# Kernel optimization log

Hardware: AMD Instinct MI355X
Metric: run time of the kernel (lower is better)

The kernel has to match this reference:

```python
import jax, jax.numpy as jnp
import numpy as np
from jax import lax

DIM = 256
HEADS = 8
B, H, W = 8, 128, 128
EPS_LN = 1e-5
EPS_NORM = 1e-12


def _ln(x, w, b):
    # WithBias LayerNorm over channel dim, x: [b,c,h,w]
    mu = x.mean(axis=1, keepdims=True)
    var = ((x - mu) ** 2).mean(axis=1, keepdims=True)
    return (x - mu) / jnp.sqrt(var + EPS_LN) * w[None, :, None, None] + b[None, :, None, None]


def _conv1x1(x, w, b):
    # w: [out,in]
    return jnp.einsum('bchw,oc->bohw', x, w) + b[None, :, None, None]


def _dwconv3(x, w, b=None):
    # depthwise 3x3, w: [C,1,3,3]
    c = x.shape[1]
    y = lax.conv_general_dilated(x, w, (1, 1), 'SAME',
                                 dimension_numbers=('NCHW', 'OIHW', 'NCHW'),
                                 feature_group_count=c)
    if b is not None:
        y = y + b[None, :, None, None]
    return y


def setup_inputs() -> dict:
    key = jax.random.key(0)
    ks = jax.random.split(key, 10)
    s = 0.02
    return {
        'x': jax.random.normal(ks[0], (B, DIM, H, W), jnp.float32),
        'hx': jax.random.normal(ks[1], (B, DIM, H, W), jnp.float32),
        'ln1_w': jnp.ones((DIM,), jnp.float32),
        'ln1_b': jnp.zeros((DIM,), jnp.float32),
        'ln2_w': jnp.ones((DIM,), jnp.float32),
        'ln2_b': jnp.zeros((DIM,), jnp.float32),
        'q_w': jax.random.normal(ks[2], (DIM, DIM), jnp.float32) * s,
        'q_b': jnp.zeros((DIM,), jnp.float32),
        'q_dw_w': jax.random.normal(ks[3], (DIM, 1, 3, 3), jnp.float32) * s,
        'q_dw_b': jnp.zeros((DIM,), jnp.float32),
        'kv_w': jax.random.normal(ks[4], (2 * DIM, DIM), jnp.float32) * s,
        'kv_b': jnp.zeros((2 * DIM,), jnp.float32),
        'kv_dw_w': jax.random.normal(ks[5], (2 * DIM, 1, 3, 3), jnp.float32) * s,
        'kv_dw_b': jnp.zeros((2 * DIM,), jnp.float32),
        'ao_w': jax.random.normal(ks[6], (DIM, DIM), jnp.float32) * s,
        'ao_b': jnp.zeros((DIM,), jnp.float32),
        'pe1_w': jax.random.normal(ks[7], (DIM, 1, 3, 3), jnp.float32) * s,
        'pe2_w': jax.random.normal(ks[8], (DIM, 1, 3, 3), jnp.float32) * s,
        'temperature': jnp.ones((HEADS, 1, 1), jnp.float32),
    }


def reference(x, hx, ln1_w, ln1_b, ln2_w, ln2_b, q_w, q_b, q_dw_w, q_dw_b,
              kv_w, kv_b, kv_dw_w, kv_dw_b, ao_w, ao_b, pe1_w, pe2_w, temperature):
    b, c, h, w = hx.shape
    q = _dwconv3(_conv1x1(_ln(x, ln1_w, ln1_b), q_w, q_b), q_dw_w, q_dw_b)
    kv = _dwconv3(_conv1x1(_ln(hx, ln2_w, ln2_b), kv_w, kv_b), kv_dw_w, kv_dw_b)
    k, v = jnp.split(kv, 2, axis=1)
    # positional embedding branch: dwconv -> GELU -> dwconv (no bias)
    p_emb = _dwconv3(jax.nn.gelu(_dwconv3(v, pe1_w)), pe2_w)
    hd = c // HEADS
    # [b, head, hd, hw]
    qh = q.reshape(b, HEADS, hd, h * w)
    kh = k.reshape(b, HEADS, hd, h * w)
    vh = v.reshape(b, HEADS, hd, h * w)
    qh = qh / jnp.maximum(jnp.linalg.norm(qh, axis=-1, keepdims=True), EPS_NORM)
    kh = kh / jnp.maximum(jnp.linalg.norm(kh, axis=-1, keepdims=True), EPS_NORM)
    attn = jnp.einsum('bhcn,bhdn->bhcd', qh, kh) * temperature[None]
    attn = jax.nn.softmax(attn, axis=-1)
    out = jnp.einsum('bhcd,bhdn->bhcn', attn, vh).reshape(b, c, h, w)
    return _conv1x1(out, ao_w, ao_b) + p_emb + hx
```

## Files before the change

### kernel.cpp

```cpp
#include <hip/hip_runtime.h>
#include <cstdio>
#include <cstdint>

typedef unsigned short u16;
typedef short short8 __attribute__((ext_vector_type(8)));
typedef float floatx4 __attribute__((ext_vector_type(4)));

#define NPIX 16384
#define DIM 256

__device__ inline float bf2f(u16 v) {
    return __uint_as_float(((uint32_t)v) << 16);
}
__device__ inline u16 f2bf(float f) {
    uint32_t u = __float_as_uint(f);
    u += 0x7fffu + ((u >> 16) & 1u);
    return (u16)(u >> 16);
}
__device__ inline float gelu_tanh(float x) {
    float x3 = x * x * x;
    return 0.5f * x * (1.f + tanhf(0.7978845608028654f * (x + 0.044715f * x3)));
}
__device__ inline void load8(const u16* p, size_t idx, int isf32, float out[8]) {
    if (isf32) {
        const float4* f = (const float4*)((const float*)p + idx);
        float4 a = f[0], b = f[1];
        out[0] = a.x; out[1] = a.y; out[2] = a.z; out[3] = a.w;
        out[4] = b.x; out[5] = b.y; out[6] = b.z; out[7] = b.w;
    } else {
        uint4 d = *(const uint4*)(p + idx);
        u16 v[8]; *(uint4*)v = d;
#pragma unroll
        for (int j = 0; j < 8; ++j) out[j] = bf2f(v[j]);
    }
}

__global__ __launch_bounds__(256)
void detect_dtype(const u16* __restrict__ x, int* __restrict__ flag) {
    __shared__ int sh[256];
    int t = threadIdx.x;
    const uint32_t* w = (const uint32_t*)x;
    int cnt = 0;
    for (int i = t; i < 4096; i += 256) {
        int e = (w[i] >> 7) & 0xFF;
        if (e >= 110 && e <= 134) cnt++;
    }
    sh[t] = cnt;
    __syncthreads();
    if (t == 0) {
        int s = 0;
        for (int i = 0; i < 256; ++i) s += sh[i];
        *flag = (s < 2048) ? 1 : 0;
    }
}

struct WArgs {
    const void* src[17];
    int off[17];
    int n[17];
};
__global__ __launch_bounds__(256)
void convert_params(WArgs a, const int* __restrict__ flag, u16* __restrict__ dst) {
    int isf32 = *flag;
    int w = blockIdx.y;
    const void* s = a.src[w];
    u16* d = dst + a.off[w];
    int n = a.n[w];
    for (int i = blockIdx.x * 256 + threadIdx.x; i < n; i += gridDim.x * 256)
        d[i] = isf32 ? f2bf(((const float*)s)[i]) : ((const u16*)s)[i];
}

__global__ __launch_bounds__(256)
void ln_stats(const u16* __restrict__ x, const int* __restrict__ flag,
              float* __restrict__ mu, float* __restrict__ rstd) {
    int isf32 = *flag;
    int g = blockIdx.x * 256 + threadIdx.x;
    int b = g >> 14, n = g & (NPIX - 1);
    float s = 0.f, s2 = 0.f;
    if (isf32) {
        const float* p = (const float*)x + (size_t)b * DIM * NPIX + n;
        for (int c = 0; c < DIM; ++c) { float v = p[(size_t)c * NPIX]; s += v; s2 += v * v; }
    } else {
        const u16* p = x + (size_t)b * DIM * NPIX + n;
        for (int c = 0; c < DIM; ++c) { float v = bf2f(p[(size_t)c * NPIX]); s += v; s2 += v * v; }
    }
    float m = s * (1.f / 256.f);
    float var = s2 * (1.f / 256.f) - m * m;
    mu[g] = m;
    rstd[g] = rsqrtf(var + 1e-5f);
}

__global__ __launch_bounds__(256)
void ln_transpose(const u16* __restrict__ x, const int* __restrict__ flag,
                  const float* __restrict__ mu, const float* __restrict__ rstd,
                  const u16* __restrict__ lnw, const u16* __restrict__ lnb,
                  u16* __restrict__ xt) {
    int isf32 = *flag;
    __shared__ u16 T[64][72];
    int b = blockIdx.x >> 8;
    int n0 = (blockIdx.x & 255) * 64;
    int c0 = blockIdx.y * 64;
    int t = threadIdx.x;
#pragma unroll
    for (int l = 0; l < 2; ++l) {
        int idx = t + l * 256;
        int cl = idx >> 3, nch = (idx & 7) * 8;
        float vals[8];
        load8(x, ((size_t)(b * DIM + c0 + cl)) * NPIX + n0 + nch, isf32, vals);
        float w = bf2f(lnw[c0 + cl]), bb = bf2f(lnb[c0 + cl]);
#pragma unroll
        for (int j = 0; j < 8; ++j) {
            int g = b * NPIX + n0 + nch + j;
            float v = (vals[j] - mu[g]) * rstd[g] * w + bb;
            T[nch + j][cl] = f2bf(v);
        }
    }
    __syncthreads();
#pragma unroll
    for (int l = 0; l < 2; ++l) {
        int idx = t + l * 256;
        int nl = idx >> 3, cch = (idx & 7) * 8;
        uint4 d = *(const uint4*)&T[nl][cch];
        *(uint4*)(xt + (size_t)(b * NPIX + n0 + nl) * DIM + c0 + cch) = d;
    }
}

template <int HAS_ADD>
__global__ __launch_bounds__(256)
void gemm_bf16(const u16* __restrict__ A, const u16* __restrict__ Bw,
               const u16* __restrict__ bias, const u16* __restrict__ addt,
               u16* __restrict__ C, int ldc) {
    __shared__ u16 As[128][40];
    __shared__ u16 Bs[128][40];
    const int m0 = blockIdx.x * 128;
    const int n0 = blockIdx.y * 128;
    const int t = threadIdx.x;
    const int lane = t & 63;
    const int wid = t >> 6;
    const int wm = (wid >> 1) * 64;
    const int wn = (wid & 1) * 64;
    const int frow = lane & 15;
    const int koff = (lane >> 4) * 8;
    floatx4 acc[4][4] = {};
    for (int k0 = 0; k0 < 256; k0 += 32) {
#pragma unroll
        for (int l = 0; l < 2; ++l) {
            int idx = t + l * 256;
            int r = idx >> 2, ch = (idx & 3) * 8;
            *(uint4*)&As[r][ch] = *(const uint4*)(A + (size_t)(m0 + r) * 256 + k0 + ch);
            *(uint4*)&Bs[r][ch] = *(const uint4*)(Bw + (size_t)(n0 + r) * 256 + k0 + ch);
        }
        __syncthreads();
        short8 af[4], bfr[4];
#pragma unroll
        for (int i = 0; i < 4; ++i) {
            af[i] = *(const short8*)&As[wm + i * 16 + frow][koff];
            bfr[i] = *(const short8*)&Bs[wn + i * 16 + frow][koff];
        }
#pragma unroll
        for (int i = 0; i < 4; ++i)
#pragma unroll
            for (int j = 0; j < 4; ++j)
                acc[i][j] = __builtin_amdgcn_mfma_f32_16x16x32_bf16(af[i], bfr[j], acc[i][j], 0, 0, 0);
        __syncthreads();
    }
    const int col = lane & 15;
    const int r0 = (lane >> 4) * 4;
#pragma unroll
    for (int j = 0; j < 4; ++j) {
        int o = n0 + wn + j * 16 + col;
        float bv = bf2f(bias[o]);
#pragma unroll
        for (int i = 0; i < 4; ++i) {
#pragma unroll
            for (int r = 0; r < 4; ++r) {
                int m = m0 + wm + i * 16 + r0 + r;
                size_t off = (size_t)m * ldc + o;
                float v = acc[i][j][r] + bv;
                if (HAS_ADD) v += bf2f(addt[off]);
                C[off] = f2bf(v);
            }
        }
    }
}

__global__ __launch_bounds__(256)
void dwconv3_nhwc(const u16* __restrict__ in, int in_stride, int in_off,
                  const u16* __restrict__ w9, const u16* __restrict__ bias,
                  u16* __restrict__ out, int out_stride, int out_off,
                  int C, int do_gelu) {
    extern __shared__ float wsm[];
    int t = threadIdx.x;
    for (int i = t; i < C * 9; i += 256) {
        int c = i / 9, tap = i % 9;
        wsm[tap * C + c] = bf2f(w9[i]);
    }
    __syncthreads();
    const int tpp = C >> 3;
    const int ppb = 256 / tpp;
    int pix = blockIdx.x * ppb + t / tpp;
    int c8 = (t % tpp) * 8;
    int b = pix >> 14, n = pix & (NPIX - 1);
    int y = n >> 7, x = n & 127;
    float acc[8] = {0, 0, 0, 0, 0, 0, 0, 0};
    const u16* base = in + (size_t)(b * NPIX) * in_stride + in_off + c8;
#pragma unroll
    for (int dy = -1; dy <= 1; ++dy) {
        int yy = y + dy;
        if ((unsigned)yy >= 128u) continue;
#pragma unroll
        for (int dx = -1; dx <= 1; ++dx) {
            int xx = x + dx;
            if ((unsigned)xx >= 128u) continue;
            uint4 d = *(const uint4*)(base + (size_t)(yy * 128 + xx) * in_stride);
            u16 v[8]; *(uint4*)v = d;
            int tap = (dy + 1) * 3 + (dx + 1);
            const float4* wp = (const float4*)&wsm[tap * C + c8];
            float4 w0 = wp[0], w1 = wp[1];
            acc[0] += bf2f(v[0]) * w0.x; acc[1] += bf2f(v[1]) * w0.y;
            acc[2] += bf2f(v[2]) * w0.z; acc[3] += bf2f(v[3]) * w0.w;
            acc[4] += bf2f(v[4]) * w1.x; acc[5] += bf2f(v[5]) * w1.y;
            acc[6] += bf2f(v[6]) * w1.z; acc[7] += bf2f(v[7]) * w1.w;
        }
    }
    u16 o[8];
#pragma unroll
    for (int j = 0; j < 8; ++j) {
        float r = acc[j];
        if (bias) r += bf2f(bias[c8 + j]);
        if (do_gelu) r = gelu_tanh(r);
        o[j] = f2bf(r);
    }
    *(uint4*)(out + (size_t)pix * out_stride + out_off + c8) = *(uint4*)o;
}

__global__ __launch_bounds__(256)
void finalize_scales(const float* __restrict__ qss, const float* __restrict__ kss,
                     float* __restrict__ qsc, float* __restrict__ ksc) {
    int i = blockIdx.x * 256 + threadIdx.x;
    qsc[i] = 1.f / fmaxf(sqrtf(qss[i]), 1e-12f);
    ksc[i] = 1.f / fmaxf(sqrtf(kss[i]), 1e-12f);
}

__global__ __launch_bounds__(256)
void gram_kernel(const u16* __restrict__ qT, const u16* __restrict__ kvT,
                 float* __restrict__ Gpart, float* __restrict__ qss,
                 float* __restrict__ kss) {
    int blk = blockIdx.x;
    int b = blk >> 7, chunk = blk & 127;
    int t = threadIdx.x;
    int hbase = t & 0xE0;
    int row0 = b * NPIX + chunk * 128;
    const u16* qp = qT + (size_t)row0 * 256 + t;
    const u16* kp = kvT + (size_t)row0 * 512;
    float acc[32];
#pragma unroll
    for (int j = 0; j < 32; ++j) acc[j] = 0.f;
    float qs2 = 0.f, ks2 = 0.f;
#pragma unroll 2
    for (int r = 0; r < 128; ++r) {
        float qv = bf2f(qp[(size_t)r * 256]);
        const u16* krow = kp + (size_t)r * 512;
        float kt = bf2f(krow[t]);
        qs2 += qv * qv;
        ks2 += kt * kt;
        uint4 k0 = *(const uint4*)(krow + hbase);
        uint4 k1 = *(const uint4*)(krow + hbase + 8);
        uint4 k2 = *(const uint4*)(krow + hbase + 16);
        uint4 k3 = *(const uint4*)(krow + hbase + 24);
        u16 kv16[32];
        *(uint4*)(kv16 + 0)  = k0;
        *(uint4*)(kv16 + 8)  = k1;
        *(uint4*)(kv16 + 16) = k2;
        *(uint4*)(kv16 + 24) = k3;
#pragma unroll
        for (int j = 0; j < 32; ++j) acc[j] += qv * bf2f(kv16[j]);
    }
    float* gp = Gpart + (size_t)blk * 8192 + t * 32;
#pragma unroll
    for (int j = 0; j < 32; j += 4)
        *(float4*)(gp + j) = make_float4(acc[j], acc[j + 1], acc[j + 2], acc[j + 3]);
    atomicAdd(&qss[b * 256 + t], qs2);
    atomicAdd(&kss[b * 256 + t], ks2);
}

__global__ __launch_bounds__(1024)
void softmax32(const float* __restrict__ Gpart, const float* __restrict__ qsc,
               const float* __restrict__ ksc, const u16* __restrict__ temp,
               float* __restrict__ attn) {
    int bh = blockIdx.x;
    int b = bh >> 3, h = bh & 7;
    int t = threadIdx.x;
    int i = t >> 5, j = t & 31;
    const float* gp = Gpart + (size_t)b * 128 * 8192 + (size_t)((h * 32 + i) * 32 + j);
    float s0 = 0.f, s1 = 0.f, s2 = 0.f, s3 = 0.f;
    for (int p = 0; p < 128; p += 4) {
        s0 += gp[(size_t)p * 8192];
        s1 += gp[(size_t)(p + 1) * 8192];
        s2 += gp[(size_t)(p + 2) * 8192];
        s3 += gp[(size_t)(p + 3) * 8192];
    }
    float qs = qsc[b * 256 + h * 32 + i];
    float ks = ksc[b * 256 + h * 32 + j];
    float tm = bf2f(temp[h]);
    float v = ((s0 + s1) + (s2 + s3)) * qs * ks * tm;
    float m = v;
    for (int s = 16; s; s >>= 1) m = fmaxf(m, __shfl_xor(m, s, 32));
    float e = __expf(v - m);
    float sum = e;
    for (int s = 16; s; s >>= 1) sum += __shfl_xor(sum, s, 32);
    attn[((size_t)(b * 8 + h) * 32 + i) * 32 + j] = e / sum;
}

__global__ __launch_bounds__(256)
void attnv_kernel(const float* __restrict__ attn, const u16* __restrict__ kvT,
                  u16* __restrict__ outT) {
    __shared__ float at[8][32][33];
    __shared__ u16 vs[8][256];
    int b = blockIdx.x >> 7, chunk = blockIdx.x & 127;
    int t = threadIdx.x;
    for (int idx = t; idx < 8192; idx += 256) {
        int hh = idx >> 10, rem = idx & 1023;
        at[hh][rem >> 5][rem & 31] = attn[(size_t)b * 8192 + idx];
    }
    int h = t >> 5, i = t & 31;
    int row0 = b * NPIX + chunk * 128;
    int rr = t >> 5, cc = (t & 31) * 8;
    for (int r8 = 0; r8 < 128; r8 += 8) {
        __syncthreads();
        *(uint4*)&vs[rr][cc] = *(const uint4*)(kvT + (size_t)(row0 + r8 + rr) * 512 + 256 + cc);
        __syncthreads();
#pragma unroll
        for (int r = 0; r < 8; ++r) {
            float a = 0.f;
#pragma unroll
            for (int j = 0; j < 32; j += 4) {
                uint2 vd = *(const uint2*)&vs[r][h * 32 + j];
                u16 v4[4]; *(uint2*)v4 = vd;
                a += at[h][i][j]     * bf2f(v4[0]);
                a += at[h][i][j + 1] * bf2f(v4[1]);
                a += at[h][i][j + 2] * bf2f(v4[2]);
                a += at[h][i][j + 3] * bf2f(v4[3]);
            }
            outT[(size_t)(row0 + r8 + r) * 256 + t] = f2bf(a);
        }
    }
}

__global__ __launch_bounds__(256)
void final_out(const u16* __restrict__ Fp, const u16* __restrict__ hx,
               const int* __restrict__ flag, u16* __restrict__ out) {
    int isf32 = *flag;
    __shared__ u16 T[64][72];
    int b = blockIdx.x >> 8;
    int n0 = (blockIdx.x & 255) * 64;
    int c0 = blockIdx.y * 64;
    int t = threadIdx.x;
#pragma unroll
    for (int l = 0; l < 2; ++l) {
        int idx = t + l * 256;
        int nl = idx >> 3, cch = (idx & 7) * 8;
        *(uint4*)&T[nl][cch] = *(const uint4*)(Fp + (size_t)(b * NPIX + n0 + nl) * 256 + c0 + cch);
    }
    __syncthreads();
#pragma unroll
    for (int l = 0; l < 2; ++l) {
        int idx = t + l * 256;
        int cl = idx >> 3, nch = (idx & 7) * 8;
        size_t g = (size_t)(b * DIM + c0 + cl) * NPIX + n0 + nch;
        float hv[8];
        load8(hx, g, isf32, hv);
        float r[8];
#pragma unroll
        for (int j = 0; j < 8; ++j) r[j] = bf2f(T[nch + j][cl]) + hv[j];
        if (isf32) {
            float* o = (float*)out + g;
            *(float4*)o       = make_float4(r[0], r[1], r[2], r[3]);
            *(float4*)(o + 4) = make_float4(r[4], r[5], r[6], r[7]);
        } else {
            u16 ov[8];
#pragma unroll
            for (int j = 0; j < 8; ++j) ov[j] = f2bf(r[j]);
            *(uint4*)(out + g) = *(uint4*)ov;
        }
    }
}

__global__ void ws_marker(u16* out) {
    if (threadIdx.x < 64) ((uint32_t*)out)[threadIdx.x] = 0x46402400u;
}

extern "C" void kernel_launch(void* const* d_in, const int* in_sizes, int n_in,
                              void* d_out, int out_size, void* d_ws, size_t ws_size,
                              hipStream_t stream) {
    const u16* x    = (const u16*)d_in[0];
    const u16* hx   = (const u16*)d_in[1];
    u16* outp = (u16*)d_out;

    char* ws = (char*)d_ws;
    float* F = (float*)ws;
    float* mu_x   = F;
    float* rstd_x = F + 131072;
    float* mu_h   = F + 262144;
    float* rstd_h = F + 393216;
    float* qss    = F + 524288;
    float* kss    = F + 526336;
    float* qsc    = F + 528384;
    float* ksc    = F + 530432;
    float* attn   = F + 598016;
    int*   dflag  = (int*)(F + 663552);
    u16*   W      = (u16*)(ws + 2752512);
    u16* R1 = (u16*)(ws + (((size_t)4)   << 20));
    u16* R2 = (u16*)(ws + (((size_t)68)  << 20));
    u16* R3 = (u16*)(ws + (((size_t)132) << 20));
    u16* R4 = (u16*)(ws + (((size_t)260) << 20));
    float* Gpart = (float*)R2;

    size_t need = ((size_t)388) << 20;
    if (ws_size < need) {
        ws_marker<<<1, 64, 0, stream>>>(outp);
        return;
    }

    const int O_QW = 0, O_KVW = 65536, O_AOW = 196608, O_QB = 262144, O_KVB = 262400,
              O_AOB = 262912, O_LN1W = 263168, O_LN1B = 263424, O_LN2W = 263680,
              O_LN2B = 263936, O_QDWW = 264192, O_QDWB = 266496, O_KVDWW = 266752,
              O_KVDWB = 271360, O_PE1 = 271872, O_PE2 = 274176, O_TEMP = 276480;

    WArgs wa;
    const int srcidx[17] = {6, 10, 14, 7, 11, 15, 2, 3, 4, 5, 8, 9, 12, 13, 16, 17, 18};
    const int offs[17]   = {O_QW, O_KVW, O_AOW, O_QB, O_KVB, O_AOB, O_LN1W, O_LN1B,
                            O_LN2W, O_LN2B, O_QDWW, O_QDWB, O_KVDWW, O_KVDWB,
                            O_PE1, O_PE2, O_TEMP};
    const int ns[17]     = {65536, 131072, 65536, 256, 512, 256, 256, 256, 256, 256,
                            2304, 256, 4608, 512, 2304, 2304, 8};
    for (int i = 0; i < 17; ++i) { wa.src[i] = d_in[srcidx[i]]; wa.off[i] = offs[i]; wa.n[i] = ns[i]; }

    detect_dtype<<<1, 256, 0, stream>>>(x, dflag);
    convert_params<<<dim3(16, 17), 256, 0, stream>>>(wa, dflag, W);

    hipMemsetAsync(ws + (size_t)524288 * 4, 0, (size_t)(532480 - 524288) * 4, stream);

    ln_stats<<<512, 256, 0, stream>>>(x, dflag, mu_x, rstd_x);
    ln_stats<<<512, 256, 0, stream>>>(hx, dflag, mu_h, rstd_h);

    ln_transpose<<<dim3(2048, 4), 256, 0, stream>>>(x, dflag, mu_x, rstd_x, W + O_LN1W, W + O_LN1B, R1);
    gemm_bf16<0><<<dim3(1024, 2), 256, 0, stream>>>(R1, W + O_QW, W + O_QB, nullptr, R2, 256);

    ln_transpose<<<dim3(2048, 4), 256, 0, stream>>>(hx, dflag, mu_h, rstd_h, W + O_LN2W, W + O_LN2B, R1);
    gemm_bf16<0><<<dim3(1024, 4), 256, 0, stream>>>(R1, W + O_KVW, W + O_KVB, nullptr, R3, 512);

    dwconv3_nhwc<<<16384, 256, 9 * 256 * 4, stream>>>(R2, 256, 0, W + O_QDWW, W + O_QDWB, R1, 256, 0, 256, 0);
    dwconv3_nhwc<<<32768, 256, 9 * 512 * 4, stream>>>(R3, 512, 0, W + O_KVDWW, W + O_KVDWB, R4, 512, 0, 512, 0);

    gram_kernel<<<1024, 256, 0, stream>>>(R1, R4, Gpart, qss, kss);
    finalize_scales<<<8, 256, 0, stream>>>(qss, kss, qsc, ksc);
    softmax32<<<64, 1024, 0, stream>>>(Gpart, qsc, ksc, W + O_TEMP, attn);
    attnv_kernel<<<1024, 256, 0, stream>>>(attn, R4, R2);

    dwconv3_nhwc<<<16384, 256, 9 * 256 * 4, stream>>>(R4, 512, 256, W + O_PE1, nullptr, R3, 256, 0, 256, 1);
    dwconv3_nhwc<<<16384, 256, 9 * 256 * 4, stream>>>(R3, 256, 0, W + O_PE2, nullptr, R1, 256, 0, 256, 0);

    gemm_bf16<1><<<dim3(1024, 2), 256, 0, stream>>>(R2, W + O_AOW, W + O_AOB, R1, R3, 256);
    final_out<<<dim3(2048, 4), 256, 0, stream>>>(R3, hx, dflag, outp);
}
```

Before: 1.387 ms.

## Register-tile depthwise 3x3 conv over 4 pixels per thread with templated weights

Replaces the one-pixel-per-thread depthwise conv with a templated kernel where each thread computes 4 horizontally adjacent pixels. Each loaded input column is reused across up to 3 taps, which cuts global loads per output. Weights move from shared memory into registers, which removes the shared-memory fill and barrier. Bias and GELU become compile-time flags, and GELU uses an exp/rcp sigmoid form instead of tanhf. The cost is higher register pressure from 72 weight floats plus 32 accumulators, which may lower occupancy.

Result: faster. 1.314 ms (-5.3%).

```diff
diff --git a/kernel.cpp b/kernel.cpp
--- a/kernel.cpp
+++ b/kernel.cpp
@@ -17,9 +17,10 @@
     u += 0x7fffu + ((u >> 16) & 1u);
     return (u16)(u >> 16);
 }
-__device__ inline float gelu_tanh(float x) {
+__device__ inline float gelu_fast(float x) {
     float x3 = x * x * x;
-    return 0.5f * x * (1.f + tanhf(0.7978845608028654f * (x + 0.044715f * x3)));
+    float z2 = 1.5957691216057308f * (x + 0.044715f * x3);
+    return x * __builtin_amdgcn_rcpf(1.f + __expf(-z2));
 }
 __device__ inline void load8(const u16* p, size_t idx, int isf32, float out[8]) {
     if (isf32) {
@@ -184,54 +185,82 @@
     }
 }
 
-__global__ __launch_bounds__(256)
-void dwconv3_nhwc(const u16* __restrict__ in, int in_stride, int in_off,
-                  const u16* __restrict__ w9, const u16* __restrict__ bias,
-                  u16* __restrict__ out, int out_stride, int out_off,
-                  int C, int do_gelu) {
-    extern __shared__ float wsm[];
-    int t = threadIdx.x;
-    for (int i = t; i < C * 9; i += 256) {
-        int c = i / 9, tap = i % 9;
-        wsm[tap * C + c] = bf2f(w9[i]);
-    }
-    __syncthreads();
-    const int tpp = C >> 3;
-    const int ppb = 256 / tpp;
-    int pix = blockIdx.x * ppb + t / tpp;
-    int c8 = (t % tpp) * 8;
-    int b = pix >> 14, n = pix & (NPIX - 1);
-    int y = n >> 7, x = n & 127;
-    float acc[8] = {0, 0, 0, 0, 0, 0, 0, 0};
-    const u16* base = in + (size_t)(b * NPIX) * in_stride + in_off + c8;
+template <int C, int HAS_BIAS, int DO_GELU>
+__global__ __launch_bounds__(256)
+void dwconv3_reg(const u16* __restrict__ in, int in_stride, int in_off,
+                 const u16* __restrict__ w9, const u16* __restrict__ bias,
+                 u16* __restrict__ out, int out_stride, int out_off) {
+    constexpr int TPP = C / 8;
+    constexpr int GRP = 256 / TPP;
+    constexpr int XSEG = 128 / (GRP * 4);
+    int t = threadIdx.x;
+    int cl = t & (TPP - 1);
+    int g = t / TPP;
+    int c8 = cl * 8;
+    int blk = blockIdx.x;
+    int xs = blk & (XSEG - 1);
+    int tmp = blk / XSEG;
+    int y = tmp & 127;
+    int b = tmp >> 7;
+    int x0 = xs * (GRP * 4) + g * 4;
+
+    u16 wl[72];
+#pragma unroll
+    for (int i = 0; i < 9; ++i)
+        *((uint4*)wl + i) = *((const uint4*)(w9 + c8 * 9) + i);
+    float wgt[9][8];
+#pragma unroll
+    for (int tap = 0; tap < 9; ++tap)
+#pragma unroll
+        for (int j = 0; j < 8; ++j)
+            wgt[tap][j] = bf2f(wl[j * 9 + tap]);
+
+    float acc[4][8] = {};
 #pragma unroll
     for (int dy = -1; dy <= 1; ++dy) {
         int yy = y + dy;
         if ((unsigned)yy >= 128u) continue;
-#pragma unroll
-        for (int dx = -1; dx <= 1; ++dx) {
-            int xx = x + dx;
-            if ((unsigned)xx >= 128u) continue;
-            uint4 d = *(const uint4*)(base + (size_t)(yy * 128 + xx) * in_stride);
+        const u16* rp = in + (size_t)(b * NPIX + yy * 128) * in_stride + in_off + c8;
+#pragma unroll
+        for (int ci = 0; ci < 6; ++ci) {
+            int cc = x0 - 1 + ci;
+            if ((unsigned)cc >= 128u) continue;
+            uint4 d = *(const uint4*)(rp + (size_t)cc * in_stride);
             u16 v[8]; *(uint4*)v = d;
-            int tap = (dy + 1) * 3 + (dx + 1);
-            const float4* wp = (const float4*)&wsm[tap * C + c8];
-            float4 w0 = wp[0], w1 = wp[1];
-            acc[0] += bf2f(v[0]) * w0.x; acc[1] += bf2f(v[1]) * w0.y;
-            acc[2] += bf2f(v[2]) * w0.z; acc[3] += bf2f(v[3]) * w0.w;
-            acc[4] += bf2f(v[4]) * w1.x; acc[5] += bf2f(v[5]) * w1.y;
-            acc[6] += bf2f(v[6]) * w1.z; acc[7] += bf2f(v[7]) * w1.w;
-        }
-    }
-    u16 o[8];
-#pragma unroll
-    for (int j = 0; j < 8; ++j) {
-        float r = acc[j];
-        if (bias) r += bf2f(bias[c8 + j]);
-        if (do_gelu) r = gelu_tanh(r);
-        o[j] = f2bf(r);
-    }
-    *(uint4*)(out + (size_t)pix * out_stride + out_off + c8) = *(uint4*)o;
+            float fv[8];
+#pragma unroll
+            for (int j = 0; j < 8; ++j) fv[j] = bf2f(v[j]);
+#pragma unroll
+            for (int dx = -1; dx <= 1; ++dx) {
+                int p = ci - 1 - dx;
+                if (p < 0 || p > 3) continue;
+                int tap = (dy + 1) * 3 + (dx + 1);
+#pragma unroll
+                for (int j = 0; j < 8; ++j) acc[p][j] += fv[j] * wgt[tap][j];
+            }
+        }
+    }
+
+    float bi[8];
+    if (HAS_BIAS) {
+        uint4 bd = *(const uint4*)(bias + c8);
+        u16 bv[8]; *(uint4*)bv = bd;
+#pragma unroll
+        for (int j = 0; j < 8; ++j) bi[j] = bf2f(bv[j]);
+    }
+    u16* op = out + (size_t)(b * NPIX + y * 128 + x0) * out_stride + out_off + c8;
+#pragma unroll
+    for (int p = 0; p < 4; ++p) {
+        u16 o[8];
+#pragma unroll
+        for (int j = 0; j < 8; ++j) {
+            float r = acc[p][j];
+            if (HAS_BIAS) r += bi[j];
+            if (DO_GELU) r = gelu_fast(r);
+            o[j] = f2bf(r);
+        }
+        *(uint4*)(op + (size_t)p * out_stride) = *(uint4*)o;
+    }
 }
 
 __global__ __launch_bounds__(256)
@@ -450,16 +479,16 @@
     ln_transpose<<<dim3(2048, 4), 256, 0, stream>>>(hx, dflag, mu_h, rstd_h, W + O_LN2W, W + O_LN2B, R1);
     gemm_bf16<0><<<dim3(1024, 4), 256, 0, stream>>>(R1, W + O_KVW, W + O_KVB, nullptr, R3, 512);
 
-    dwconv3_nhwc<<<16384, 256, 9 * 256 * 4, stream>>>(R2, 256, 0, W + O_QDWW, W + O_QDWB, R1, 256, 0, 256, 0);
-    dwconv3_nhwc<<<32768, 256, 9 * 512 * 4, stream>>>(R3, 512, 0, W + O_KVDWW, W + O_KVDWB, R4, 512, 0, 512, 0);
+    dwconv3_reg<256, 1, 0><<<4096, 256, 0, stream>>>(R2, 256, 0, W + O_QDWW, W + O_QDWB, R1, 256, 0);
+    dwconv3_reg<512, 1, 0><<<8192, 256, 0, stream>>>(R3, 512, 0, W + O_KVDWW, W + O_KVDWB, R4, 512, 0);
 
     gram_kernel<<<1024, 256, 0, stream>>>(R1, R4, Gpart, qss, kss);
     finalize_scales<<<8, 256, 0, stream>>>(qss, kss, qsc, ksc);
     softmax32<<<64, 1024, 0, stream>>>(Gpart, qsc, ksc, W + O_TEMP, attn);
     attnv_kernel<<<1024, 256, 0, stream>>>(attn, R4, R2);
 
-    dwconv3_nhwc<<<16384, 256, 9 * 256 * 4, stream>>>(R4, 512, 256, W + O_PE1, nullptr, R3, 256, 0, 256, 1);
-    dwconv3_nhwc<<<16384, 256, 9 * 256 * 4, stream>>>(R3, 256, 0, W + O_PE2, nullptr, R1, 256, 0, 256, 0);
+    dwconv3_reg<256, 0, 1><<<4096, 256, 0, stream>>>(R4, 512, 256, W + O_PE1, nullptr, R3, 256, 0);
+    dwconv3_reg<256, 0, 0><<<4096, 256, 0, stream>>>(R3, 256, 0, W + O_PE2, nullptr, R1, 256, 0);
 
     gemm_bf16<1><<<dim3(1024, 2), 256, 0, stream>>>(R2, W + O_AOW, W + O_AOB, R1, R3, 256);
     final_out<<<dim3(2048, 4), 256, 0, stream>>>(R3, hx, dflag, outp);
```
